# Kernel optimization log

Hardware: AMD Instinct MI355X
Metric: run time of the kernel (lower is better)

The kernel has to match this reference:

```python
import jax, jax.numpy as jnp
import numpy as np

PAD = 4
STRIDE = 1
KSIZE = 9

def setup_inputs() -> dict:
    key = jax.random.key(0)
    k1, k2, k3 = jax.random.split(key, 3)
    x = jax.random.normal(k1, (64, 64, 1024), dtype=jnp.float32)          # (B, C_in, W_in)
    weights = jax.random.uniform(k2, (1024, 64, 64, 9), dtype=jnp.float32)  # (W_out, C_out, C_in, K)
    bias = jax.random.uniform(k3, (64, 1024), dtype=jnp.float32)           # (C_out, W_out)
    return {"x": x, "weights": weights, "bias": bias}

def reference(x, weights, bias):
    W_out, C_out, C_in, K = weights.shape
    B = x.shape[0]
    xp = jnp.pad(x, ((0, 0), (0, 0), (PAD, PAD)))
    # gather patches: (B, C_in, W_out, K)
    idx = jnp.arange(W_out)[:, None] * STRIDE + jnp.arange(K)[None, :]
    patches = xp[:, :, idx]
    # per-position unshared conv: (B, W_out, C_out)
    res = jnp.einsum('bcwk,wock->bwo', patches, weights)
    # faithful to original: flatten (W_out, C_out) then reshape as (C_out, W_out)
    out = res.reshape(B, C_out, W_out)
    out = out + bias[None, :, :]
    return out
```

## Files before the change

kernel.cpp:

```cpp
#include <hip/hip_runtime.h>
#include <hip/hip_bf16.h>


typedef __bf16 bf16x8 __attribute__((ext_vector_type(8)));
typedef float  f32x4  __attribute__((ext_vector_type(4)));

#define NK    576
#define LDAP  296
#define NCH   18
#define PFD   6
#define XT_SLABS 1032
#define XT_BYTES ((size_t)XT_SLABS * 4096 * 2)

#define LGKM_BAR() asm volatile("s_waitcnt lgkmcnt(0)\n\ts_barrier" ::: "memory")

__global__ __launch_bounds__(256)
void xt_transpose_kernel(const float* __restrict__ x, __bf16* __restrict__ xt) {
    const int tid = threadIdx.x;
    if (blockIdx.x >= 256) {
        const int s    = blockIdx.x - 256;
        const int slab = (s < 4) ? s : (1024 + s);
        f32x4* p = reinterpret_cast<f32x4*>(xt + (size_t)slab * 4096);
        const f32x4 z = (f32x4){0.f, 0.f, 0.f, 0.f};
        p[tid] = z;
        p[256 + tid] = z;
        return;
    }
    __shared__ float T[64][17];
    const int b      = blockIdx.x >> 2;
    const int p_base = (blockIdx.x & 3) * 256;
    const int cr = tid >> 2;
    const int pq = (tid & 3) * 4;
    const int pl = tid >> 3;
    const int cg = tid & 7;

    for (int tile = 0; tile < 16; ++tile) {
        const int p0 = p_base + tile * 16;
        f32x4 v = *reinterpret_cast<const f32x4*>(x + (((size_t)(b * 64 + cr)) << 10) + p0 + pq);
        if (tile) __syncthreads();
        T[cr][pq + 0] = v[0];
        T[cr][pq + 1] = v[1];
        T[cr][pq + 2] = v[2];
        T[cr][pq + 3] = v[3];
        __syncthreads();
        if (tid < 128) {
            bf16x8 o8;
            #pragma unroll
            for (int i = 0; i < 8; ++i) o8[i] = (__bf16)T[cg * 8 + i][pl];
            *reinterpret_cast<bf16x8*>(xt + (size_t)(p0 + pl + 4) * 4096 + b * 64 + cg * 8) = o8;
        }
    }
}

__global__ __launch_bounds__(256, 4)
void lc1d_main_kernel(const __bf16* __restrict__ xt,
                      const float* __restrict__ wts,
                      const float* __restrict__ bias,
                      float* __restrict__ out) {
    __shared__ __bf16 Alds[64][LDAP];

    const int orig = blockIdx.x;
    const int w    = ((orig & 7) << 7) | (orig >> 3);

    const int tid  = threadIdx.x;
    const int lane = tid & 63;
    const int wv   = tid >> 6;
    const int m16  = lane & 15;
    const int ko   = (lane >> 4) * 8;
    const int o    = wv * 16 + m16;

    const float* wbase = wts + (size_t)w * (64 * NK) + (size_t)o * NK + ko;

    const int sb  = tid >> 2;
    const int sc8 = (tid & 3) * 8;
    const __bf16* xtb = xt + (size_t)w * 4096 + sb * 64 + sc8;

    bf16x8 v[9];
    #pragma unroll
    for (int t = 0; t < 9; ++t)
        v[t] = *reinterpret_cast<const bf16x8*>(xtb + (size_t)t * 4096);

    f32x4 wr0[PFD], wr1[PFD];
    #pragma unroll
    for (int p = 0; p < PFD; ++p) {
        wr0[p] = *reinterpret_cast<const f32x4*>(wbase + p * 32);
        wr1[p] = *reinterpret_cast<const f32x4*>(wbase + p * 32 + 4);
    }

    {
        __bf16* dst = &Alds[sb][sc8 * 9];
        #pragma unroll
        for (int q = 0; q < 9; ++q) {
            bf16x8 u;
            #pragma unroll
            for (int j = 0; j < 8; ++j) { int n = q * 8 + j; u[j] = v[n % 9][n / 9]; }
            *reinterpret_cast<bf16x8*>(dst + q * 8) = u;
        }
    }
    LGKM_BAR();

    f32x4 acc[4];
    #pragma unroll
    for (int i = 0; i < 4; ++i) acc[i] = (f32x4){0.f, 0.f, 0.f, 0.f};

    #pragma unroll
    for (int t = 0; t < 9; ++t)
        v[t] = *reinterpret_cast<const bf16x8*>(xtb + 32 + (size_t)t * 4096);

    #pragma unroll
    for (int it = 0; it < 9; ++it) {
        const int s = it % PFD;
        f32x4 u0 = wr0[s], u1 = wr1[s];
        wr0[s] = *reinterpret_cast<const f32x4*>(wbase + (it + PFD) * 32);
        wr1[s] = *reinterpret_cast<const f32x4*>(wbase + (it + PFD) * 32 + 4);
        bf16x8 bf;
        #pragma unroll
        for (int j = 0; j < 4; ++j) { bf[j] = (__bf16)u0[j]; bf[j + 4] = (__bf16)u1[j]; }
        const int kk0 = it * 32;
        #pragma unroll
        for (int bt = 0; bt < 4; ++bt) {
            bf16x8 af = *reinterpret_cast<const bf16x8*>(&Alds[bt * 16 + m16][kk0 + ko]);
            acc[bt] = __builtin_amdgcn_mfma_f32_16x16x32_bf16(af, bf, acc[bt], 0, 0, 0);
        }
    }

    LGKM_BAR();

    {
        __bf16* dst = &Alds[sb][sc8 * 9];
        #pragma unroll
        for (int q = 0; q < 9; ++q) {
            bf16x8 u;
            #pragma unroll
            for (int j = 0; j < 8; ++j) { int n = q * 8 + j; u[j] = v[n % 9][n / 9]; }
            *reinterpret_cast<bf16x8*>(dst + q * 8) = u;
        }
    }
    LGKM_BAR();

    #pragma unroll
    for (int it = 9; it < NCH; ++it) {
        const int s = it % PFD;
        f32x4 u0 = wr0[s], u1 = wr1[s];
        if (it + PFD < NCH) {
            wr0[s] = *reinterpret_cast<const f32x4*>(wbase + (it + PFD) * 32);
            wr1[s] = *reinterpret_cast<const f32x4*>(wbase + (it + PFD) * 32 + 4);
        }
        bf16x8 bf;
        #pragma unroll
        for (int j = 0; j < 4; ++j) { bf[j] = (__bf16)u0[j]; bf[j + 4] = (__bf16)u1[j]; }
        const int kk0 = (it - 9) * 32;
        #pragma unroll
        for (int bt = 0; bt < 4; ++bt) {
            bf16x8 af = *reinterpret_cast<const bf16x8*>(&Alds[bt * 16 + m16][kk0 + ko]);
            acc[bt] = __builtin_amdgcn_mfma_f32_16x16x32_bf16(af, bf, acc[bt], 0, 0, 0);
        }
    }

    const float bv = bias[w * 64 + o];
    const int r0 = (lane >> 4) * 4;
    float* outp = out + (size_t)w * 64 + o;
    #pragma unroll
    for (int bt = 0; bt < 4; ++bt) {
        #pragma unroll
        for (int r = 0; r < 4; ++r) {
            int b = bt * 16 + r0 + r;
            outp[(size_t)b * 65536] = acc[bt][r] + bv;
        }
    }
}

__global__ __launch_bounds__(256, 4)
void lc1d_fallback_kernel(const float* __restrict__ x,
                          const float* __restrict__ wts,
                          const float* __restrict__ bias,
                          float* __restrict__ out) {
    __shared__ __bf16 Alds[64][LDAP];
    const int w    = blockIdx.x;
    const int tid  = threadIdx.x;
    const int lane = tid & 63;
    const int wv   = tid >> 6;
    const int m16  = lane & 15;
    const int ko   = (lane >> 4) * 8;
    const int o    = wv * 16 + m16;
    const float* wbase = wts + (size_t)w * (64 * NK) + (size_t)o * NK + ko;
    const int xbase  = w - 4;
    const int a0     = xbase & ~3;
    const int d      = xbase - a0;
    const int rowsel = tid >> 2;
    const int sl     = tid & 3;
    const int p0     = a0 + sl * 4;
    const bool inb   = ((unsigned)p0 < 1024u);

    f32x4 acc[4];
    #pragma unroll
    for (int i = 0; i < 4; ++i) acc[i] = (f32x4){0.f, 0.f, 0.f, 0.f};

    #pragma unroll
    for (int ph = 0; ph < 2; ++ph) {
        f32x4 wr[18];
        const float* wp = wbase + ph * 288;
        #pragma unroll
        for (int it = 0; it < 9; ++it) {
            wr[2 * it]     = *reinterpret_cast<const f32x4*>(wp + it * 32);
            wr[2 * it + 1] = *reinterpret_cast<const f32x4*>(wp + it * 32 + 4);
        }
        if (ph) __syncthreads();
        #pragma unroll 4
        for (int i = 0; i < 32; ++i) {
            int R  = i * 64 + rowsel;
            int c  = R & 31;
            int b  = R >> 5;
            int cc = ph * 32 + c;
            f32x4 vv = (f32x4){0.f, 0.f, 0.f, 0.f};
            if (inb) vv = *reinterpret_cast<const f32x4*>(x + (((size_t)(b * 64 + cc)) << 10) + p0);
            __bf16* dst = &Alds[b][c * 9];
            #pragma unroll
            for (int j = 0; j < 4; ++j) {
                int t = sl * 4 + j - d;
                if (t >= 0 && t <= 8) dst[t] = (__bf16)vv[j];
            }
        }
        __syncthreads();
        #pragma unroll
        for (int it = 0; it < 9; ++it) {
            bf16x8 bf;
            #pragma unroll
            for (int j = 0; j < 4; ++j) { bf[j] = (__bf16)wr[2 * it][j]; bf[j + 4] = (__bf16)wr[2 * it + 1][j]; }
            const int kk0 = it * 32;
            #pragma unroll
            for (int bt = 0; bt < 4; ++bt) {
                bf16x8 af = *reinterpret_cast<const bf16x8*>(&Alds[bt * 16 + m16][kk0 + ko]);
                acc[bt] = __builtin_amdgcn_mfma_f32_16x16x32_bf16(af, bf, acc[bt], 0, 0, 0);
            }
        }
    }
    const float bv = bias[w * 64 + o];
    const int r0 = (lane >> 4) * 4;
    float* outp = out + (size_t)w * 64 + o;
    #pragma unroll
    for (int bt = 0; bt < 4; ++bt) {
        #pragma unroll
        for (int r = 0; r < 4; ++r) {
            int b = bt * 16 + r0 + r;
            outp[(size_t)b * 65536] = acc[bt][r] + bv;
        }
    }
}

extern "C" void kernel_launch(void* const* d_in, const int* in_sizes, int n_in,
                              void* d_out, int out_size, void* d_ws, size_t ws_size,
                              hipStream_t stream) {
    const float* x    = (const float*)d_in[0];
    const float* wts  = (const float*)d_in[1];
    const float* bias = (const float*)d_in[2];
    float* out = (float*)d_out;

    if (ws_size >= XT_BYTES) {
        __bf16* xt = (__bf16*)d_ws;
        xt_transpose_kernel<<<dim3(264), dim3(256), 0, stream>>>(x, xt);
        lc1d_main_kernel<<<dim3(1024), dim3(256), 0, stream>>>(xt, wts, bias, out);
    } else {
        lc1d_fallback_kernel<<<dim3(1024), dim3(256), 0, stream>>>(x, wts, bias, out);
    }
}
```

Measured before the change: 43.43 us.

## Spread transpose over more blocks and hoist bias load in main kernel

The transpose kernel previously used 256 blocks that each looped over 16 tiles with barriers. It now uses 2048 blocks, each handling a single 64x32 tile in one pass, to raise parallelism and remove the serial tile loop. The bias load in the main kernel is moved to the start so its latency overlaps with compute. In exchange there are more block launches, and each transposed element is still read once.

```diff
diff --git a/kernel.cpp b/kernel.cpp
--- a/kernel.cpp
+++ b/kernel.cpp
@@ -17,8 +17,8 @@
 __global__ __launch_bounds__(256)
 void xt_transpose_kernel(const float* __restrict__ x, __bf16* __restrict__ xt) {
     const int tid = threadIdx.x;
-    if (blockIdx.x >= 256) {
-        const int s    = blockIdx.x - 256;
+    if (blockIdx.x >= 2048) {
+        const int s    = blockIdx.x - 2048;
         const int slab = (s < 4) ? s : (1024 + s);
         f32x4* p = reinterpret_cast<f32x4*>(xt + (size_t)slab * 4096);
         const f32x4 z = (f32x4){0.f, 0.f, 0.f, 0.f};
@@ -26,30 +26,25 @@
         p[256 + tid] = z;
         return;
     }
-    __shared__ float T[64][17];
-    const int b      = blockIdx.x >> 2;
-    const int p_base = (blockIdx.x & 3) * 256;
-    const int cr = tid >> 2;
-    const int pq = (tid & 3) * 4;
+    __shared__ float T[64][33];
+    const int b  = blockIdx.x >> 5;
+    const int p0 = (blockIdx.x & 31) * 32;
+
+    const int c = tid >> 2;
+    const int q = tid & 3;
+    const float* src = x + (((size_t)(b * 64 + c)) << 10) + p0 + q * 8;
+    f32x4 v0 = *reinterpret_cast<const f32x4*>(src);
+    f32x4 v1 = *reinterpret_cast<const f32x4*>(src + 4);
+    #pragma unroll
+    for (int i = 0; i < 4; ++i) { T[c][q * 8 + i] = v0[i]; T[c][q * 8 + 4 + i] = v1[i]; }
+    __syncthreads();
+
     const int pl = tid >> 3;
     const int cg = tid & 7;
-
-    for (int tile = 0; tile < 16; ++tile) {
-        const int p0 = p_base + tile * 16;
-        f32x4 v = *reinterpret_cast<const f32x4*>(x + (((size_t)(b * 64 + cr)) << 10) + p0 + pq);
-        if (tile) __syncthreads();
-        T[cr][pq + 0] = v[0];
-        T[cr][pq + 1] = v[1];
-        T[cr][pq + 2] = v[2];
-        T[cr][pq + 3] = v[3];
-        __syncthreads();
-        if (tid < 128) {
-            bf16x8 o8;
-            #pragma unroll
-            for (int i = 0; i < 8; ++i) o8[i] = (__bf16)T[cg * 8 + i][pl];
-            *reinterpret_cast<bf16x8*>(xt + (size_t)(p0 + pl + 4) * 4096 + b * 64 + cg * 8) = o8;
-        }
-    }
+    bf16x8 o8;
+    #pragma unroll
+    for (int i = 0; i < 8; ++i) o8[i] = (__bf16)T[cg * 8 + i][pl];
+    *reinterpret_cast<bf16x8*>(xt + (size_t)(p0 + pl + 4) * 4096 + b * 64 + cg * 8) = o8;
 }
 
 __global__ __launch_bounds__(256, 4)
@@ -71,6 +66,8 @@
 
     const float* wbase = wts + (size_t)w * (64 * NK) + (size_t)o * NK + ko;
 
+    const float bv = bias[w * 64 + o];
+
     const int sb  = tid >> 2;
     const int sc8 = (tid & 3) * 8;
     const __bf16* xtb = xt + (size_t)w * 4096 + sb * 64 + sc8;
@@ -90,11 +87,11 @@
     {
         __bf16* dst = &Alds[sb][sc8 * 9];
         #pragma unroll
-        for (int q = 0; q < 9; ++q) {
+        for (int qq = 0; qq < 9; ++qq) {
             bf16x8 u;
             #pragma unroll
-            for (int j = 0; j < 8; ++j) { int n = q * 8 + j; u[j] = v[n % 9][n / 9]; }
-            *reinterpret_cast<bf16x8*>(dst + q * 8) = u;
+            for (int j = 0; j < 8; ++j) { int n = qq * 8 + j; u[j] = v[n % 9][n / 9]; }
+            *reinterpret_cast<bf16x8*>(dst + qq * 8) = u;
         }
     }
     LGKM_BAR();
@@ -129,11 +126,11 @@
     {
         __bf16* dst = &Alds[sb][sc8 * 9];
         #pragma unroll
-        for (int q = 0; q < 9; ++q) {
+        for (int qq = 0; qq < 9; ++qq) {
             bf16x8 u;
             #pragma unroll
-            for (int j = 0; j < 8; ++j) { int n = q * 8 + j; u[j] = v[n % 9][n / 9]; }
-            *reinterpret_cast<bf16x8*>(dst + q * 8) = u;
+            for (int j = 0; j < 8; ++j) { int n = qq * 8 + j; u[j] = v[n % 9][n / 9]; }
+            *reinterpret_cast<bf16x8*>(dst + qq * 8) = u;
         }
     }
     LGKM_BAR();
@@ -157,7 +154,6 @@
         }
     }
 
-    const float bv = bias[w * 64 + o];
     const int r0 = (lane >> 4) * 4;
     float* outp = out + (size_t)w * 64 + o;
     #pragma unroll
@@ -258,7 +254,7 @@
 
     if (ws_size >= XT_BYTES) {
         __bf16* xt = (__bf16*)d_ws;
-        xt_transpose_kernel<<<dim3(264), dim3(256), 0, stream>>>(x, xt);
+        xt_transpose_kernel<<<dim3(2056), dim3(256), 0, stream>>>(x, xt);
         lc1d_main_kernel<<<dim3(1024), dim3(256), 0, stream>>>(xt, wts, bias, out);
     } else {
         lc1d_fallback_kernel<<<dim3(1024), dim3(256), 0, stream>>>(x, wts, bias, out);
```

After: 39.77 us. -8.4%, faster.
